# Optimization experiments

Measured on AMD Instinct MI355X. Metric: run time of the kernel, lower is better.

## Reference

```python
import jax, jax.numpy as jnp
import numpy as np

N_NODES = 50000
N_EDGES = 800000
D_IN = 64   # input_dimension + 1
D_HID = 64


def _gcn_conv(x, src, dst, W, b, deg_isqrt):
    # PyG GCNConv: X' = D^{-1/2} (A + I) D^{-1/2} X W + b
    h = x @ W  # [N, H]
    norm = (deg_isqrt[src] * deg_isqrt[dst])[:, None]  # [E, 1]
    agg = jax.ops.segment_sum(h[src] * norm, dst, num_segments=x.shape[0])
    # self-loop contribution: norm_ii = deg_isqrt[i]^2
    agg = agg + h * (deg_isqrt * deg_isqrt)[:, None]
    return agg + b


def setup_inputs() -> dict:
    key = jax.random.key(0)
    ks = jax.random.split(key, 8)
    x = jax.random.normal(ks[0], (N_NODES, D_IN), dtype=jnp.float32)
    edge_index = jax.random.randint(ks[1], (2, N_EDGES), 0, N_NODES, dtype=jnp.int32)
    s = 1.0 / np.sqrt(D_HID)
    W0 = jax.random.normal(ks[2], (D_IN, D_HID), dtype=jnp.float32) * s
    b0 = jnp.zeros((D_HID,), dtype=jnp.float32)
    W1 = jax.random.normal(ks[3], (D_HID, D_HID), dtype=jnp.float32) * s
    b1 = jnp.zeros((D_HID,), dtype=jnp.float32)
    W2 = jax.random.normal(ks[4], (D_HID, D_HID), dtype=jnp.float32) * s
    b2 = jnp.zeros((D_HID,), dtype=jnp.float32)
    Wout = jax.random.normal(ks[5], (D_HID, 1), dtype=jnp.float32) * s
    bout = jnp.zeros((1,), dtype=jnp.float32)
    return {"x": x, "edge_index": edge_index, "W0": W0, "b0": b0,
            "W1": W1, "b1": b1, "W2": W2, "b2": b2,
            "Wout": Wout, "bout": bout}


def reference(x, edge_index, W0, b0, W1, b1, W2, b2, Wout, bout):
    src, dst = edge_index[0], edge_index[1]
    n = x.shape[0]
    # degree with self-loop (edge weight 1.0 each)
    deg = jnp.zeros((n,), x.dtype).at[dst].add(1.0) + 1.0
    deg_isqrt = jax.lax.rsqrt(deg)
    h = jax.nn.relu(_gcn_conv(x, src, dst, W0, b0, deg_isqrt))
    h = jax.nn.relu(_gcn_conv(h, src, dst, W1, b1, deg_isqrt))
    h = jax.nn.relu(_gcn_conv(h, src, dst, W2, b2, deg_isqrt))
    return h @ Wout + bout  # [N, 1]
```

## Files before the change

kernel.cpp:

```cpp
#include <hip/hip_runtime.h>
#include <hip/hip_bf16.h>

#define D 64
#define N_NODES 50000
#define N_EDGES 800000

__global__ void hist_k(const int* __restrict__ dst, int* __restrict__ cnt, int E) {
    int i = blockIdx.x * blockDim.x + threadIdx.x;
    if (i < E) atomicAdd(&cnt[dst[i]], 1);
}

__global__ void scan1_k(const int* __restrict__ cnt, int* __restrict__ off,
                        int* __restrict__ bsum, float* __restrict__ dis, int N) {
    __shared__ int sh[256];
    int t = threadIdx.x;
    int i = blockIdx.x * 256 + t;
    int v = (i < N) ? cnt[i] : 0;
    sh[t] = v;
    __syncthreads();
#pragma unroll
    for (int d = 1; d < 256; d <<= 1) {
        int u = (t >= d) ? sh[t - d] : 0;
        __syncthreads();
        sh[t] += u;
        __syncthreads();
    }
    if (i < N) {
        off[i] = sh[t] - v;
        dis[i] = rsqrtf((float)v + 1.0f);
    }
    if (t == 255) bsum[blockIdx.x] = sh[255];
}

__global__ void scan2_k(int* __restrict__ bsum, int nb) {
    __shared__ int sh[256];
    int t = threadIdx.x;
    int v = (t < nb) ? bsum[t] : 0;
    sh[t] = v;
    __syncthreads();
#pragma unroll
    for (int d = 1; d < 256; d <<= 1) {
        int u = (t >= d) ? sh[t - d] : 0;
        __syncthreads();
        sh[t] += u;
        __syncthreads();
    }
    if (t < nb) bsum[t] = sh[t] - v;
}

__global__ void scan3_k(int* __restrict__ off, const int* __restrict__ bsum,
                        int* __restrict__ cursor, int N, int E) {
    int i = blockIdx.x * 256 + threadIdx.x;
    if (i < N) {
        int o = off[i] + bsum[blockIdx.x];
        off[i] = o;
        cursor[i] = o;
    }
    if (i == 0) off[N] = E;
}

__global__ void fused0_k(const float* __restrict__ X, const float* __restrict__ W,
                         const float* __restrict__ dis, float* __restrict__ H,
                         const int* __restrict__ src, const int* __restrict__ dst,
                         int* __restrict__ cursor, int* __restrict__ esrc,
                         int N, int E, int gemmBlocks) {
    __shared__ float Ws[D * D];
    __shared__ float Xs[4][D];
    int bid = blockIdx.x;
    if (bid < gemmBlocks) {
        for (int i = threadIdx.x; i < D * D; i += blockDim.x) Ws[i] = W[i];
        __syncthreads();
        int r = threadIdx.x >> 6;
        int c = threadIdx.x & 63;
        for (int row0 = bid * 4; row0 < N; row0 += gemmBlocks * 4) {
            int row = row0 + r;
            if (row < N) Xs[r][c] = X[(size_t)row * D + c];
            __syncthreads();
            if (row < N) {
                float acc = 0.0f;
#pragma unroll
                for (int k = 0; k < D; ++k) acc = fmaf(Xs[r][k], Ws[k * D + c], acc);
                H[(size_t)row * D + c] = acc * dis[row];
            }
            __syncthreads();
        }
    } else {
        int fb = bid - gemmBlocks;
        int nfb = gridDim.x - gemmBlocks;
        for (int i = fb * 256 + threadIdx.x; i < E; i += nfb * 256) {
            int pos = atomicAdd(&cursor[dst[i]], 1);
            esrc[pos] = src[i];
        }
    }
}

template <int FINAL>
__global__ void layer_k(const float4* __restrict__ Hs4, const int* __restrict__ off,
                        const int* __restrict__ esrc, const float* __restrict__ dis,
                        const float* __restrict__ bias, const float* __restrict__ W,
                        const float* __restrict__ bout, float* __restrict__ outp, int N) {
    int wid = (blockIdx.x * blockDim.x + threadIdx.x) >> 6;
    int lane = threadIdx.x & 63;
    int grp = lane >> 4;
    int l16 = lane & 15;
    int c = lane;

    float Wc[64];
    if (!FINAL) {
#pragma unroll
        for (int k = 0; k < 64; ++k) Wc[k] = W[k * 64 + c];
    }
    float4 b4 = ((const float4*)bias)[l16];

    if (wid >= N) return;

    int beg = off[wid], end = off[wid + 1];
    float4 acc = make_float4(0.f, 0.f, 0.f, 0.f);
    if (grp == 0) acc = Hs4[(size_t)wid * 16 + l16];

    int j = beg + grp;
    for (; j + 12 < end; j += 16) {
        int s0 = esrc[j], s1 = esrc[j + 4], s2 = esrc[j + 8], s3 = esrc[j + 12];
        float4 v0 = Hs4[(size_t)s0 * 16 + l16];
        float4 v1 = Hs4[(size_t)s1 * 16 + l16];
        float4 v2 = Hs4[(size_t)s2 * 16 + l16];
        float4 v3 = Hs4[(size_t)s3 * 16 + l16];
        acc.x += (v0.x + v1.x) + (v2.x + v3.x);
        acc.y += (v0.y + v1.y) + (v2.y + v3.y);
        acc.z += (v0.z + v1.z) + (v2.z + v3.z);
        acc.w += (v0.w + v1.w) + (v2.w + v3.w);
    }
    for (; j < end; j += 4) {
        int s = esrc[j];
        float4 v = Hs4[(size_t)s * 16 + l16];
        acc.x += v.x; acc.y += v.y; acc.z += v.z; acc.w += v.w;
    }
#pragma unroll
    for (int m = 16; m <= 32; m <<= 1) {
        acc.x += __shfl_xor(acc.x, m, 64);
        acc.y += __shfl_xor(acc.y, m, 64);
        acc.z += __shfl_xor(acc.z, m, 64);
        acc.w += __shfl_xor(acc.w, m, 64);
    }
    float dv = dis[wid];
    float4 h4;
    h4.x = fmaxf(fmaf(acc.x, dv, b4.x), 0.f);
    h4.y = fmaxf(fmaf(acc.y, dv, b4.y), 0.f);
    h4.z = fmaxf(fmaf(acc.z, dv, b4.z), 0.f);
    h4.w = fmaxf(fmaf(acc.w, dv, b4.w), 0.f);

    if (FINAL) {
        float4 w4 = ((const float4*)W)[l16];
        float p = h4.x * w4.x + h4.y * w4.y + h4.z * w4.z + h4.w * w4.w;
        p += __shfl_xor(p, 1, 64);
        p += __shfl_xor(p, 2, 64);
        p += __shfl_xor(p, 4, 64);
        p += __shfl_xor(p, 8, 64);
        if (lane == 0) outp[wid] = p + bout[0];
    } else {
        float o = 0.f;
#pragma unroll
        for (int ch = 0; ch < 16; ++ch) {
            float hx = __shfl(h4.x, ch, 64);
            float hy = __shfl(h4.y, ch, 64);
            float hz = __shfl(h4.z, ch, 64);
            float hw = __shfl(h4.w, ch, 64);
            o = fmaf(hx, Wc[4 * ch + 0], o);
            o = fmaf(hy, Wc[4 * ch + 1], o);
            o = fmaf(hz, Wc[4 * ch + 2], o);
            o = fmaf(hw, Wc[4 * ch + 3], o);
        }
        outp[(size_t)wid * 64 + c] = o * dv;
    }
}

extern "C" void kernel_launch(void* const* d_in, const int* in_sizes, int n_in,
                              void* d_out, int out_size, void* d_ws, size_t ws_size,
                              hipStream_t stream) {
    const float* x    = (const float*)d_in[0];
    const int*   ei   = (const int*)d_in[1];
    const float* W0   = (const float*)d_in[2];
    const float* b0   = (const float*)d_in[3];
    const float* W1   = (const float*)d_in[4];
    const float* b1   = (const float*)d_in[5];
    const float* W2   = (const float*)d_in[6];
    const float* b2   = (const float*)d_in[7];
    const float* Wout = (const float*)d_in[8];
    const float* bout = (const float*)d_in[9];
    float* out = (float*)d_out;

    const int N = N_NODES, E = N_EDGES;
    const int* src = ei;
    const int* dst = ei + E;

    char* ws = (char*)d_ws;
    int*   cnt    = (int*)(ws);
    int*   off    = (int*)(ws + (256u << 10));
    int*   cursor = (int*)(ws + (512u << 10));
    float* dis    = (float*)(ws + (768u << 10));
    int*   bsum   = (int*)(ws + (990u << 10));
    int*   esrc   = (int*)(ws + (1u << 20));
    float* bufA   = (float*)(ws + (5u << 20));
    float* bufB   = (float*)(ws + (18u << 20));

    dim3 blk(256);
    const int NB = (N + 255) / 256;
    dim3 gN(NB);
    dim3 gE((E + 255) / 256);
    dim3 gWave((N * 64 + 255) / 256);
    const int GEMM_BLOCKS = 2048;
    const int FILL_BLOCKS = 1024;

    hipMemsetAsync(cnt, 0, (size_t)N * sizeof(int), stream);
    hist_k<<<gE, blk, 0, stream>>>(dst, cnt, E);
    scan1_k<<<gN, blk, 0, stream>>>(cnt, off, bsum, dis, N);
    scan2_k<<<1, blk, 0, stream>>>(bsum, NB);
    scan3_k<<<gN, blk, 0, stream>>>(off, bsum, cursor, N, E);

    fused0_k<<<dim3(GEMM_BLOCKS + FILL_BLOCKS), blk, 0, stream>>>(
        x, W0, dis, bufA, src, dst, cursor, esrc, N, E, GEMM_BLOCKS);

    layer_k<0><<<gWave, blk, 0, stream>>>((const float4*)bufA, off, esrc, dis,
                                          b0, W1, nullptr, bufB, N);
    layer_k<0><<<gWave, blk, 0, stream>>>((const float4*)bufB, off, esrc, dis,
                                          b1, W2, nullptr, bufA, N);
    layer_k<1><<<gWave, blk, 0, stream>>>((const float4*)bufA, off, esrc, dis,
                                          b2, Wout, bout, out, N);
}
```

Baseline: 345.9 us.

## Transpose weights once and do per-node GEMV via LDS broadcast with float4 loads

A small kernel transposes W0, W1 and W2 into workspace once per call. A shared gemv64 helper then handles the dense step in both the first-layer GEMM and the hidden layers. Each wave stores its 64-wide row in LDS, and each lane reads a contiguous transposed weight row as float4 loads. This drops the 64-float per-thread register copy of W and the 64 shuffles per node in layer_k, and removes the shared-memory staging and block barriers from the fused0 GEMM path. The cost is that weights are re-read from cache for every node instead of sitting in registers, plus one extra kernel launch.

```diff
diff --git a/kernel.cpp b/kernel.cpp
--- a/kernel.cpp
+++ b/kernel.cpp
@@ -59,30 +59,49 @@
     if (i == 0) off[N] = E;
 }
 
-__global__ void fused0_k(const float* __restrict__ X, const float* __restrict__ W,
+__global__ void transpose_k(const float* __restrict__ W0, const float* __restrict__ W1,
+                            const float* __restrict__ W2, float* __restrict__ WT0,
+                            float* __restrict__ WT1, float* __restrict__ WT2) {
+    const float* Wsrc = (blockIdx.x == 0) ? W0 : (blockIdx.x == 1) ? W1 : W2;
+    float* Wdst = (blockIdx.x == 0) ? WT0 : (blockIdx.x == 1) ? WT1 : WT2;
+    for (int i = threadIdx.x; i < D * D; i += 256) {
+        Wdst[(i & 63) * 64 + (i >> 6)] = Wsrc[i];
+    }
+}
+
+__device__ __forceinline__ float gemv64(float4 v4, const float4* __restrict__ WT4,
+                                        float* __restrict__ hsh, int lane, int grp, int l16) {
+    if (grp == 0) ((float4*)hsh)[l16] = v4;
+    float o = 0.f;
+#pragma unroll
+    for (int i = 0; i < 16; ++i) {
+        float4 hb = ((const float4*)hsh)[i];
+        float4 wt = WT4[lane * 16 + i];
+        o = fmaf(hb.x, wt.x, o);
+        o = fmaf(hb.y, wt.y, o);
+        o = fmaf(hb.z, wt.z, o);
+        o = fmaf(hb.w, wt.w, o);
+    }
+    return o;
+}
+
+__global__ void fused0_k(const float4* __restrict__ X4, const float4* __restrict__ WT0_4,
                          const float* __restrict__ dis, float* __restrict__ H,
                          const int* __restrict__ src, const int* __restrict__ dst,
                          int* __restrict__ cursor, int* __restrict__ esrc,
                          int N, int E, int gemmBlocks) {
-    __shared__ float Ws[D * D];
-    __shared__ float Xs[4][D];
+    __shared__ float hsh[4][D];
     int bid = blockIdx.x;
     if (bid < gemmBlocks) {
-        for (int i = threadIdx.x; i < D * D; i += blockDim.x) Ws[i] = W[i];
-        __syncthreads();
-        int r = threadIdx.x >> 6;
-        int c = threadIdx.x & 63;
-        for (int row0 = bid * 4; row0 < N; row0 += gemmBlocks * 4) {
-            int row = row0 + r;
-            if (row < N) Xs[r][c] = X[(size_t)row * D + c];
-            __syncthreads();
-            if (row < N) {
-                float acc = 0.0f;
-#pragma unroll
-                for (int k = 0; k < D; ++k) acc = fmaf(Xs[r][k], Ws[k * D + c], acc);
-                H[(size_t)row * D + c] = acc * dis[row];
-            }
-            __syncthreads();
+        int w = threadIdx.x >> 6;
+        int lane = threadIdx.x & 63;
+        int grp = lane >> 4, l16 = lane & 15;
+        int gw = bid * 4 + w;
+        int nW = gemmBlocks * 4;
+        for (int row = gw; row < N; row += nW) {
+            float4 v4 = X4[(size_t)row * 16 + l16];
+            float o = gemv64(v4, WT0_4, hsh[w], lane, grp, l16);
+            H[(size_t)row * 64 + lane] = o * dis[row];
         }
     } else {
         int fb = bid - gemmBlocks;
@@ -97,21 +116,13 @@
 template <int FINAL>
 __global__ void layer_k(const float4* __restrict__ Hs4, const int* __restrict__ off,
                         const int* __restrict__ esrc, const float* __restrict__ dis,
-                        const float* __restrict__ bias, const float* __restrict__ W,
+                        const float* __restrict__ bias, const float4* __restrict__ WT4,
                         const float* __restrict__ bout, float* __restrict__ outp, int N) {
+    __shared__ float hsh[4][D];
     int wid = (blockIdx.x * blockDim.x + threadIdx.x) >> 6;
     int lane = threadIdx.x & 63;
     int grp = lane >> 4;
     int l16 = lane & 15;
-    int c = lane;
-
-    float Wc[64];
-    if (!FINAL) {
-#pragma unroll
-        for (int k = 0; k < 64; ++k) Wc[k] = W[k * 64 + c];
-    }
-    float4 b4 = ((const float4*)bias)[l16];
-
     if (wid >= N) return;
 
     int beg = off[wid], end = off[wid + 1];
@@ -143,6 +154,7 @@
         acc.w += __shfl_xor(acc.w, m, 64);
     }
     float dv = dis[wid];
+    float4 b4 = ((const float4*)bias)[l16];
     float4 h4;
     h4.x = fmaxf(fmaf(acc.x, dv, b4.x), 0.f);
     h4.y = fmaxf(fmaf(acc.y, dv, b4.y), 0.f);
@@ -150,27 +162,17 @@
     h4.w = fmaxf(fmaf(acc.w, dv, b4.w), 0.f);
 
     if (FINAL) {
-        float4 w4 = ((const float4*)W)[l16];
-        float p = h4.x * w4.x + h4.y * w4.y + h4.z * w4.z + h4.w * w4.w;
+        float4 w4 = ((const float4*)WT4)[l16];
+        float p = fmaf(h4.x, w4.x, fmaf(h4.y, w4.y, fmaf(h4.z, w4.z, h4.w * w4.w)));
         p += __shfl_xor(p, 1, 64);
         p += __shfl_xor(p, 2, 64);
         p += __shfl_xor(p, 4, 64);
         p += __shfl_xor(p, 8, 64);
         if (lane == 0) outp[wid] = p + bout[0];
     } else {
-        float o = 0.f;
-#pragma unroll
-        for (int ch = 0; ch < 16; ++ch) {
-            float hx = __shfl(h4.x, ch, 64);
-            float hy = __shfl(h4.y, ch, 64);
-            float hz = __shfl(h4.z, ch, 64);
-            float hw = __shfl(h4.w, ch, 64);
-            o = fmaf(hx, Wc[4 * ch + 0], o);
-            o = fmaf(hy, Wc[4 * ch + 1], o);
-            o = fmaf(hz, Wc[4 * ch + 2], o);
-            o = fmaf(hw, Wc[4 * ch + 3], o);
-        }
-        outp[(size_t)wid * 64 + c] = o * dv;
+        int w = threadIdx.x >> 6;
+        float o = gemv64(h4, WT4, hsh[w], lane, grp, l16);
+        outp[(size_t)wid * 64 + lane] = o * dv;
     }
 }
 
@@ -200,6 +202,9 @@
     float* dis    = (float*)(ws + (768u << 10));
     int*   bsum   = (int*)(ws + (990u << 10));
     int*   esrc   = (int*)(ws + (1u << 20));
+    float* WT0    = (float*)(ws + (4300u << 10));
+    float* WT1    = (float*)(ws + (4320u << 10));
+    float* WT2    = (float*)(ws + (4340u << 10));
     float* bufA   = (float*)(ws + (5u << 20));
     float* bufB   = (float*)(ws + (18u << 20));
 
@@ -216,14 +221,16 @@
     scan1_k<<<gN, blk, 0, stream>>>(cnt, off, bsum, dis, N);
     scan2_k<<<1, blk, 0, stream>>>(bsum, NB);
     scan3_k<<<gN, blk, 0, stream>>>(off, bsum, cursor, N, E);
+    transpose_k<<<dim3(3), blk, 0, stream>>>(W0, W1, W2, WT0, WT1, WT2);
 
     fused0_k<<<dim3(GEMM_BLOCKS + FILL_BLOCKS), blk, 0, stream>>>(
-        x, W0, dis, bufA, src, dst, cursor, esrc, N, E, GEMM_BLOCKS);
+        (const float4*)x, (const float4*)WT0, dis, bufA, src, dst, cursor, esrc,
+        N, E, GEMM_BLOCKS);
 
     layer_k<0><<<gWave, blk, 0, stream>>>((const float4*)bufA, off, esrc, dis,
-                                          b0, W1, nullptr, bufB, N);
+                                          b0, (const float4*)WT1, nullptr, bufB, N);
     layer_k<0><<<gWave, blk, 0, stream>>>((const float4*)bufB, off, esrc, dis,
-                                          b1, W2, nullptr, bufA, N);
+                                          b1, (const float4*)WT2, nullptr, bufA, N);
     layer_k<1><<<gWave, blk, 0, stream>>>((const float4*)bufA, off, esrc, dis,
-                                          b2, Wout, bout, out, N);
-}
+                                          b2, (const float4*)Wout, bout, out, N);
+}
```

After: 444.3 us. 28.5% more time.

## Process 16 nodes per block with quarter-wave gather and shared-memory tile GEMM

Applied to the files above, without the earlier changes.

Changes the layer kernel from one wave per node, where four lane groups split edges and then shuffle-reduce, to one quarter-wave (16 lanes) per node and 16 nodes per block. Each node's aggregated row is staged in shared memory and a float4 tile GEMM reads W from global/L1, replacing the 64-register W copy and the 64-shuffle matvec. The layer-0 GEMM uses the same tile routine with one tile per block. This cuts register pressure and shuffle work, but each node's edge gather now runs serially over 16 lanes, and the code relies on N being divisible by 16 with no bounds checks.

```diff
diff --git a/kernel.cpp b/kernel.cpp
--- a/kernel.cpp
+++ b/kernel.cpp
@@ -4,6 +4,7 @@
 #define D 64
 #define N_NODES 50000
 #define N_EDGES 800000
+#define TILE 16
 
 __global__ void hist_k(const int* __restrict__ dst, int* __restrict__ cnt, int E) {
     int i = blockIdx.x * blockDim.x + threadIdx.x;
@@ -59,31 +60,48 @@
     if (i == 0) off[N] = E;
 }
 
-__global__ void fused0_k(const float* __restrict__ X, const float* __restrict__ W,
+__device__ __forceinline__ void fma4(float4& a, float s, float4 w) {
+    a.x = fmaf(s, w.x, a.x);
+    a.y = fmaf(s, w.y, a.y);
+    a.z = fmaf(s, w.z, a.z);
+    a.w = fmaf(s, w.w, a.w);
+}
+
+__device__ __forceinline__ void tile_gemm(const float (*hbuf)[68], const float4* __restrict__ W4,
+                                          const float* __restrict__ dis, float* __restrict__ outp,
+                                          int base, int t) {
+    int lane = t & 63;
+    int cg = lane & 15;
+    int rr = (t >> 6) * 4 + (lane >> 4);
+    float4 acc = make_float4(0.f, 0.f, 0.f, 0.f);
+#pragma unroll
+    for (int kk = 0; kk < 16; ++kk) {
+        float4 hb = *(const float4*)&hbuf[rr][kk * 4];
+        fma4(acc, hb.x, W4[(kk * 4 + 0) * 16 + cg]);
+        fma4(acc, hb.y, W4[(kk * 4 + 1) * 16 + cg]);
+        fma4(acc, hb.z, W4[(kk * 4 + 2) * 16 + cg]);
+        fma4(acc, hb.w, W4[(kk * 4 + 3) * 16 + cg]);
+    }
+    float dv = dis[base + rr];
+    acc.x *= dv; acc.y *= dv; acc.z *= dv; acc.w *= dv;
+    ((float4*)outp)[(size_t)(base + rr) * 16 + cg] = acc;
+}
+
+__global__ void fused0_k(const float4* __restrict__ X4, const float4* __restrict__ W4,
                          const float* __restrict__ dis, float* __restrict__ H,
                          const int* __restrict__ src, const int* __restrict__ dst,
                          int* __restrict__ cursor, int* __restrict__ esrc,
                          int N, int E, int gemmBlocks) {
-    __shared__ float Ws[D * D];
-    __shared__ float Xs[4][D];
+    __shared__ float hbuf[TILE][68];
     int bid = blockIdx.x;
+    int t = threadIdx.x;
     if (bid < gemmBlocks) {
-        for (int i = threadIdx.x; i < D * D; i += blockDim.x) Ws[i] = W[i];
-        __syncthreads();
-        int r = threadIdx.x >> 6;
-        int c = threadIdx.x & 63;
-        for (int row0 = bid * 4; row0 < N; row0 += gemmBlocks * 4) {
-            int row = row0 + r;
-            if (row < N) Xs[r][c] = X[(size_t)row * D + c];
-            __syncthreads();
-            if (row < N) {
-                float acc = 0.0f;
-#pragma unroll
-                for (int k = 0; k < D; ++k) acc = fmaf(Xs[r][k], Ws[k * D + c], acc);
-                H[(size_t)row * D + c] = acc * dis[row];
-            }
-            __syncthreads();
-        }
+        int base = bid * TILE;
+        int r = t >> 4, ch = t & 15;
+        float4 v = X4[(size_t)(base + r) * 16 + ch];
+        *(float4*)&hbuf[r][ch * 4] = v;
+        __syncthreads();
+        tile_gemm(hbuf, W4, dis, H, base, t);
     } else {
         int fb = bid - gemmBlocks;
         int nfb = gridDim.x - gemmBlocks;
@@ -97,30 +115,22 @@
 template <int FINAL>
 __global__ void layer_k(const float4* __restrict__ Hs4, const int* __restrict__ off,
                         const int* __restrict__ esrc, const float* __restrict__ dis,
-                        const float* __restrict__ bias, const float* __restrict__ W,
+                        const float* __restrict__ bias, const float4* __restrict__ W4,
                         const float* __restrict__ bout, float* __restrict__ outp, int N) {
-    int wid = (blockIdx.x * blockDim.x + threadIdx.x) >> 6;
-    int lane = threadIdx.x & 63;
-    int grp = lane >> 4;
+    __shared__ float hbuf[TILE][68];
+    int t = threadIdx.x;
+    int lane = t & 63;
+    int w = t >> 6;
+    int g = lane >> 4;
     int l16 = lane & 15;
-    int c = lane;
-
-    float Wc[64];
-    if (!FINAL) {
-#pragma unroll
-        for (int k = 0; k < 64; ++k) Wc[k] = W[k * 64 + c];
-    }
-    float4 b4 = ((const float4*)bias)[l16];
-
-    if (wid >= N) return;
-
-    int beg = off[wid], end = off[wid + 1];
-    float4 acc = make_float4(0.f, 0.f, 0.f, 0.f);
-    if (grp == 0) acc = Hs4[(size_t)wid * 16 + l16];
-
-    int j = beg + grp;
-    for (; j + 12 < end; j += 16) {
-        int s0 = esrc[j], s1 = esrc[j + 4], s2 = esrc[j + 8], s3 = esrc[j + 12];
+    int rloc = w * 4 + g;
+    int n = blockIdx.x * TILE + rloc;
+
+    int beg = off[n], end = off[n + 1];
+    float4 acc = Hs4[(size_t)n * 16 + l16];
+    int j = beg;
+    for (; j + 3 < end; j += 4) {
+        int s0 = esrc[j], s1 = esrc[j + 1], s2 = esrc[j + 2], s3 = esrc[j + 3];
         float4 v0 = Hs4[(size_t)s0 * 16 + l16];
         float4 v1 = Hs4[(size_t)s1 * 16 + l16];
         float4 v2 = Hs4[(size_t)s2 * 16 + l16];
@@ -130,19 +140,13 @@
         acc.z += (v0.z + v1.z) + (v2.z + v3.z);
         acc.w += (v0.w + v1.w) + (v2.w + v3.w);
     }
-    for (; j < end; j += 4) {
-        int s = esrc[j];
-        float4 v = Hs4[(size_t)s * 16 + l16];
+    for (; j < end; ++j) {
+        float4 v = Hs4[(size_t)esrc[j] * 16 + l16];
         acc.x += v.x; acc.y += v.y; acc.z += v.z; acc.w += v.w;
     }
-#pragma unroll
-    for (int m = 16; m <= 32; m <<= 1) {
-        acc.x += __shfl_xor(acc.x, m, 64);
-        acc.y += __shfl_xor(acc.y, m, 64);
-        acc.z += __shfl_xor(acc.z, m, 64);
-        acc.w += __shfl_xor(acc.w, m, 64);
-    }
-    float dv = dis[wid];
+
+    float dv = dis[n];
+    float4 b4 = ((const float4*)bias)[l16];
     float4 h4;
     h4.x = fmaxf(fmaf(acc.x, dv, b4.x), 0.f);
     h4.y = fmaxf(fmaf(acc.y, dv, b4.y), 0.f);
@@ -150,27 +154,17 @@
     h4.w = fmaxf(fmaf(acc.w, dv, b4.w), 0.f);
 
     if (FINAL) {
-        float4 w4 = ((const float4*)W)[l16];
-        float p = h4.x * w4.x + h4.y * w4.y + h4.z * w4.z + h4.w * w4.w;
+        float4 w4 = ((const float4*)W4)[l16];
+        float p = fmaf(h4.x, w4.x, fmaf(h4.y, w4.y, fmaf(h4.z, w4.z, h4.w * w4.w)));
         p += __shfl_xor(p, 1, 64);
         p += __shfl_xor(p, 2, 64);
         p += __shfl_xor(p, 4, 64);
         p += __shfl_xor(p, 8, 64);
-        if (lane == 0) outp[wid] = p + bout[0];
+        if (l16 == 0) outp[n] = p + bout[0];
     } else {
-        float o = 0.f;
-#pragma unroll
-        for (int ch = 0; ch < 16; ++ch) {
-            float hx = __shfl(h4.x, ch, 64);
-            float hy = __shfl(h4.y, ch, 64);
-            float hz = __shfl(h4.z, ch, 64);
-            float hw = __shfl(h4.w, ch, 64);
-            o = fmaf(hx, Wc[4 * ch + 0], o);
-            o = fmaf(hy, Wc[4 * ch + 1], o);
-            o = fmaf(hz, Wc[4 * ch + 2], o);
-            o = fmaf(hw, Wc[4 * ch + 3], o);
-        }
-        outp[(size_t)wid * 64 + c] = o * dv;
+        *(float4*)&hbuf[rloc][l16 * 4] = h4;
+        __syncthreads();
+        tile_gemm(hbuf, W4, dis, outp, blockIdx.x * TILE, t);
     }
 }
 
@@ -207,8 +201,8 @@
     const int NB = (N + 255) / 256;
     dim3 gN(NB);
     dim3 gE((E + 255) / 256);
-    dim3 gWave((N * 64 + 255) / 256);
-    const int GEMM_BLOCKS = 2048;
+    const int TILES = N / TILE;
+    dim3 gTile(TILES);
     const int FILL_BLOCKS = 1024;
 
     hipMemsetAsync(cnt, 0, (size_t)N * sizeof(int), stream);
@@ -217,13 +211,14 @@
     scan2_k<<<1, blk, 0, stream>>>(bsum, NB);
     scan3_k<<<gN, blk, 0, stream>>>(off, bsum, cursor, N, E);
 
-    fused0_k<<<dim3(GEMM_BLOCKS + FILL_BLOCKS), blk, 0, stream>>>(
-        x, W0, dis, bufA, src, dst, cursor, esrc, N, E, GEMM_BLOCKS);
-
-    layer_k<0><<<gWave, blk, 0, stream>>>((const float4*)bufA, off, esrc, dis,
-                                          b0, W1, nullptr, bufB, N);
-    layer_k<0><<<gWave, blk, 0, stream>>>((const float4*)bufB, off, esrc, dis,
-                                          b1, W2, nullptr, bufA, N);
-    layer_k<1><<<gWave, blk, 0, stream>>>((const float4*)bufA, off, esrc, dis,
-                                          b2, Wout, bout, out, N);
-}
+    fused0_k<<<dim3(TILES + FILL_BLOCKS), blk, 0, stream>>>(
+        (const float4*)x, (const float4*)W0, dis, bufA, src, dst, cursor, esrc,
+        N, E, TILES);
+
+    layer_k<0><<<gTile, blk, 0, stream>>>((const float4*)bufA, off, esrc, dis,
+                                          b0, (const float4*)W1, nullptr, bufB, N);
+    layer_k<0><<<gTile, blk, 0, stream>>>((const float4*)bufB, off, esrc, dis,
+                                          b1, (const float4*)W2, nullptr, bufA, N);
+    layer_k<1><<<gTile, blk, 0, stream>>>((const float4*)bufA, off, esrc, dis,
+                                          b2, (const float4*)Wout, bout, out, N);
+}
```

Result: faster. 322.6 us (-6.7%).
